# Kernel optimization log

Measured on AMD Instinct MI355X. Metric: run time of the kernel, lower is better.

Reference implementation:

```python
import jax, jax.numpy as jnp
import numpy as np

B, C, N, K = 32, 1024, 2048, 64


def fps_indices(x, num):
    """Farthest-feature sampling. x: (B, N, C). Returns int32 indices (B, num).
    Deterministic start at index 0 (standard PointNet++ style loop)."""
    b, n, _ = x.shape

    def step(carry, _):
        dists, farthest = carry
        centroid = jnp.take_along_axis(x, farthest[:, None, None], axis=1)  # (B,1,C)
        d = jnp.sum((x - centroid) ** 2, axis=-1)  # (B,N)
        dists = jnp.minimum(dists, d)
        nxt = jnp.argmax(dists, axis=1).astype(jnp.int32)
        return (dists, nxt), farthest

    init = (jnp.full((b, n), 1e10, x.dtype), jnp.zeros((b,), jnp.int32))
    _, idx = jax.lax.scan(step, init, None, length=num)
    return idx.T  # (B, num)


def conv1x1(w, bias, x):
    # w: (out,in), x: (B,in,n) -> (B,out,n)
    return jnp.einsum('oi,bin->bon', w, x) + bias[:, None]


def setup_inputs() -> dict:
    key = jax.random.key(0)
    ks = jax.random.split(key, 16)
    s = 0.02
    return {
        'point_feat': jax.random.normal(ks[0], (B, C, N), jnp.float32),
        'global_feat': jax.random.normal(ks[1], (B, C), jnp.float32),
        'ps1_w': jax.random.normal(ks[2], (C, 128, K), jnp.float32) * s,
        'ps1_b': jnp.zeros((128,), jnp.float32),
        'm1c1_w': jax.random.normal(ks[3], (128, 2 * C + 128), jnp.float32) * s,
        'm1c1_b': jnp.zeros((128,), jnp.float32),
        'm1c2_w': jax.random.normal(ks[4], (128, 128), jnp.float32) * s,
        'm1c2_b': jnp.zeros((128,), jnp.float32),
        'm1sc_w': jax.random.normal(ks[5], (128, 2 * C + 128), jnp.float32) * s,
        'm1sc_b': jnp.zeros((128,), jnp.float32),
        'm2c1_w': jax.random.normal(ks[6], (64, 128), jnp.float32) * s,
        'm2c1_b': jnp.zeros((64,), jnp.float32),
        'm2c2_w': jax.random.normal(ks[7], (3, 64), jnp.float32) * s,
        'm2c2_b': jnp.zeros((3,), jnp.float32),
    }


def reference(point_feat, global_feat, ps1_w, ps1_b, m1c1_w, m1c1_b,
              m1c2_w, m1c2_b, m1sc_w, m1sc_b, m2c1_w, m2c1_b, m2c2_w, m2c2_b):
    # ffs: farthest-feature sample + gather
    xt = jnp.transpose(point_feat, (0, 2, 1))            # (B,N,C)
    idx = fps_indices(xt, K)                             # (B,K)
    feat_ffs = jnp.take_along_axis(xt, idx[:, :, None], axis=1)  # (B,K,C)
    feat_ffs = jnp.transpose(feat_ffs, (0, 2, 1))        # (B,C,K)

    # ConvTranspose1d on a length-1 input == outer product with kernel
    x1 = jnp.einsum('bi,iok->bok', global_feat, ps1_w) + ps1_b[:, None]  # (B,128,K)

    gf = jnp.broadcast_to(global_feat[:, :, None], (B, C, K))
    cat = jnp.concatenate([x1, feat_ffs, gf], axis=1)    # (B,2176,K)

    # MLP_Res
    shortcut = conv1x1(m1sc_w, m1sc_b, cat)
    h = conv1x1(m1c2_w, m1c2_b, jax.nn.relu(conv1x1(m1c1_w, m1c1_b, cat))) + shortcut

    # mlp_2
    pred = conv1x1(m2c2_w, m2c2_b, jax.nn.relu(conv1x1(m2c1_w, m2c1_b, h)))  # (B,3,K)
    return jnp.transpose(pred, (0, 2, 1))                # (B,K,3)
```

## Files before the change

### kernel.cpp

```cpp
#include <hip/hip_runtime.h>

#define BB_ 32
#define CC_ 1024
#define NN_ 2048
#define KK_ 64

typedef __bf16 bf16x8 __attribute__((ext_vector_type(8)));
typedef __bf16 bf16x2 __attribute__((ext_vector_type(2)));
typedef float f32x4 __attribute__((ext_vector_type(4)));
typedef unsigned int u32;

__device__ inline unsigned short f2bf_rn(float f) {
    unsigned u = __float_as_uint(f);
    unsigned r = (u + 0x7fffu + ((u >> 16) & 1u)) >> 16;
    return (unsigned short)r;
}

__device__ inline unsigned pack_bf16_rn(float f0, float f1) {
#if __has_builtin(__builtin_amdgcn_cvt_pk_bf16_f32)
    union { bf16x2 v; unsigned u; } x;
    x.v = __builtin_amdgcn_cvt_pk_bf16_f32(f0, f1);
    return x.u;
#else
    return (unsigned)f2bf_rn(f0) | ((unsigned)f2bf_rn(f1) << 16);
#endif
}

__device__ inline void gload16(const void* g, void* l) {
    __builtin_amdgcn_global_load_lds(
        (const __attribute__((address_space(1))) u32*)g,
        (__attribute__((address_space(3))) u32*)l, 16, 0, 0);
}

__device__ void convert_body(const float* __restrict__ X,
                             unsigned char* __restrict__ Xc, int g0,
                             int cid, int t) {
    int chunk = cid & 7;
    int kt = (cid >> 3) & 31;
    int lb = cid >> 8;
    int n = chunk * 256 + t;
    int b = g0 + lb;
    const float* Xb = X + (size_t)b * CC_ * NN_;
    unsigned char* dst = Xc + (((size_t)lb * 32 + kt) * NN_ + n) * 128;
    int sw = n & 7;
#pragma unroll
    for (int q = 0; q < 4; q++) {
        float f[8];
#pragma unroll
        for (int j = 0; j < 8; j++)
            f[j] = Xb[(size_t)(kt * 32 + q * 8 + j) * NN_ + n];
        union { unsigned u[4]; uint4 v; } hq, lq;
#pragma unroll
        for (int j2 = 0; j2 < 4; j2++) {
            float a = f[2 * j2], c = f[2 * j2 + 1];
            unsigned hp = pack_bf16_rn(a, c);
            float h0f = __uint_as_float((hp & 0xffffu) << 16);
            float h1f = __uint_as_float(hp & 0xffff0000u);
            hq.u[j2] = hp;
            lq.u[j2] = pack_bf16_rn(a - h0f, c - h1f);
        }
        int p = q ^ sw;
        *(uint4*)(dst + (p << 4)) = hq.v;
        *(uint4*)(dst + ((p ^ 4) << 4)) = lq.v;
    }
}

__global__ void convert_kernel(const float* __restrict__ X,
                               unsigned char* __restrict__ Xc, int g0) {
    convert_body(X, Xc, g0, blockIdx.x, threadIdx.x);
}

__device__ void fps_block(const float* Gb, int* idx, int b) {
    __shared__ float swv[2][4];
    __shared__ int swi[2][4];
    int t = threadIdx.x;
    float dist[8], nr[8];
#pragma unroll
    for (int r = 0; r < 8; r++) {
        nr[r] = Gb[(size_t)(t + 256 * r) * (NN_ + 1)];
        dist[r] = 1e10f;
    }
    if (t == 0) idx[b * KK_] = 0;
    int far = 0;
    for (int k = 1; k < KK_; k++) {
        float nf = Gb[(size_t)far * (NN_ + 1)];
        const float* grow = Gb + (size_t)far * NN_;
        float v = -1.f;
        int pi = 0;
#pragma unroll
        for (int r = 0; r < 8; r++) {
            float d = nr[r] + nf - 2.f * grow[t + 256 * r];
            dist[r] = fminf(dist[r], d);
            if (dist[r] > v) { v = dist[r]; pi = t + 256 * r; }
        }
#pragma unroll
        for (int off = 32; off; off >>= 1) {
            float ov = __shfl_down(v, off);
            int oi = __shfl_down(pi, off);
            if (ov > v || (ov == v && oi < pi)) { v = ov; pi = oi; }
        }
        int par = k & 1;
        if ((t & 63) == 0) { swv[par][t >> 6] = v; swi[par][t >> 6] = pi; }
        __syncthreads();
        float bv = swv[par][0];
        int bi = swi[par][0];
#pragma unroll
        for (int ww = 1; ww < 4; ww++) {
            float wv2 = swv[par][ww]; int wi2 = swi[par][ww];
            if (wv2 > bv || (wv2 == bv && wi2 < bi)) { bv = wv2; bi = wi2; }
        }
        far = bi;
        if (t == 0) idx[b * KK_ + k] = bi;
    }
}

__global__ __launch_bounds__(256, 2) void gram_fps_kernel(
    const unsigned char* __restrict__ Xc, float* __restrict__ G,
    const float* Gprev, int* __restrict__ idx, int nFps, int g0prev,
    const float* __restrict__ X, unsigned char* __restrict__ XcNext,
    int g0next, int nGram, int gs) {
    int bx = (int)blockIdx.x;
    if (bx < nFps) {
        fps_block(Gprev + (size_t)bx * NN_ * NN_, idx, g0prev + bx);
        return;
    }
    bx -= nFps;
    if (bx >= nGram) {
        convert_body(X, XcNext, g0next, bx - nGram, threadIdx.x);
        return;
    }
    int lb = bx % gs;
    int tt = bx / gs;
    int tn = (int)((sqrtf(8.f * tt + 1.f) - 1.f) * 0.5f);
    while ((tn + 1) * (tn + 2) / 2 <= tt) tn++;
    while (tn * (tn + 1) / 2 > tt) tn--;
    int tm = tt - tn * (tn + 1) / 2;
    bool diag = (tm == tn);
    int t = threadIdx.x;
    __shared__ __align__(16) unsigned char sMem[128 * 132 * 4];

    const unsigned char* XcB = Xc + (size_t)lb * 32 * NN_ * 128;
    int w = t >> 6, l = t & 63;
    int m0w = (w & 1) * 64, n0w = (w >> 1) * 64;
    int q = l >> 4, rr = l & 15;

    f32x4 zero = {0.f, 0.f, 0.f, 0.f};
    f32x4 acc[4][4];
#pragma unroll
    for (int mt = 0; mt < 4; mt++)
#pragma unroll
        for (int nt = 0; nt < 4; nt++) acc[mt][nt] = zero;

    auto stage = [&](int buf, int kt) {
        const unsigned char* Ab = XcB + ((size_t)kt * NN_ + (size_t)tm * 128) * 128;
        const unsigned char* Bb = XcB + ((size_t)kt * NN_ + (size_t)tn * 128) * 128;
        unsigned char* dA = sMem + buf * 32768;
        unsigned char* dB = dA + 16384;
#pragma unroll
        for (int r = 0; r < 4; r++) {
            gload16(Ab + r * 4096 + t * 16, dA + r * 4096 + t * 16);
            gload16(Bb + r * 4096 + t * 16, dB + r * 4096 + t * 16);
        }
    };

    stage(0, 0);
    for (int kt = 0; kt < 32; kt++) {
        int c = kt & 1;
        if (kt < 31) {
            stage(c ^ 1, kt + 1);
            asm volatile("s_waitcnt vmcnt(8)" ::: "memory");
        } else {
            asm volatile("s_waitcnt vmcnt(0)" ::: "memory");
        }
        __builtin_amdgcn_sched_barrier(0);
        __builtin_amdgcn_s_barrier();

        const unsigned char* cA = sMem + c * 32768;
        const unsigned char* cB = cA + 16384;
        bf16x8 ah[4], al[4], bh[4], bl[4];
#pragma unroll
        for (int mt = 0; mt < 4; mt++) {
            int ra = m0w + mt * 16 + rr;
            int pa = q ^ (ra & 7);
            ah[mt] = *(const bf16x8*)(cA + ra * 128 + (pa << 4));
            al[mt] = *(const bf16x8*)(cA + ra * 128 + ((pa ^ 4) << 4));
            int rb = n0w + mt * 16 + rr;
            int pb = q ^ (rb & 7);
            bh[mt] = *(const bf16x8*)(cB + rb * 128 + (pb << 4));
            bl[mt] = *(const bf16x8*)(cB + rb * 128 + ((pb ^ 4) << 4));
        }
#pragma unroll
        for (int mt = 0; mt < 4; mt++)
#pragma unroll
            for (int nt = 0; nt < 4; nt++) {
                acc[mt][nt] = __builtin_amdgcn_mfma_f32_16x16x32_bf16(ah[mt], bh[nt], acc[mt][nt], 0, 0, 0);
                acc[mt][nt] = __builtin_amdgcn_mfma_f32_16x16x32_bf16(ah[mt], bl[nt], acc[mt][nt], 0, 0, 0);
                acc[mt][nt] = __builtin_amdgcn_mfma_f32_16x16x32_bf16(al[mt], bh[nt], acc[mt][nt], 0, 0, 0);
            }
        __builtin_amdgcn_s_barrier();
    }

    float* Gb = G + (size_t)lb * NN_ * NN_;
    int i0 = tm * 128, j0 = tn * 128;
    int cc = l & 15;
    float* tb = (float*)sMem;
#pragma unroll
    for (int mt = 0; mt < 4; mt++)
#pragma unroll
        for (int nt = 0; nt < 4; nt++)
#pragma unroll
            for (int r = 0; r < 4; r++) {
                int gi = m0w + mt * 16 + q * 4 + r;
                int gj = n0w + nt * 16 + cc;
                float val = acc[mt][nt][r];
                Gb[(size_t)(i0 + gi) * NN_ + j0 + gj] = val;
                if (!diag) tb[gj * 132 + gi] = val;
            }
    if (!diag) {
        __syncthreads();
#pragma unroll
        for (int m = 0; m < 16; m++) {
            int f = t + 256 * m;
            int jj = f >> 5, sg = f & 31;
            float4 v4 = *(const float4*)(tb + jj * 132 + sg * 4);
            *(float4*)(&Gb[(size_t)(j0 + jj) * NN_ + i0 + sg * 4]) = v4;
        }
    }
}

__global__ void x1_fps_kernel(const float* __restrict__ gf, const float* __restrict__ w,
                              const float* __restrict__ bias, float* __restrict__ cat,
                              const float* Gprev, int* __restrict__ idx,
                              int g0prev, int nFps) {
    if ((int)blockIdx.x < nFps) {
        fps_block(Gprev + (size_t)blockIdx.x * NN_ * NN_, idx, g0prev + blockIdx.x);
        return;
    }
    int bid = blockIdx.x - nFps;
    int t = threadIdx.x;
    int okg = bid & 31, bg = bid >> 5;
    int ok = okg * 256 + t;
    int o = ok >> 6, k = ok & 63;
    float acc[8];
#pragma unroll
    for (int j = 0; j < 8; j++) acc[j] = 0.f;
    const float* g = gf + (size_t)(bg * 8) * CC_;
    for (int i = 0; i < CC_; i++) {
        float wv = w[(size_t)(i * 128 + o) * KK_ + k];
#pragma unroll
        for (int j = 0; j < 8; j++) acc[j] += g[j * CC_ + i] * wv;
    }
    float bv = bias[o];
#pragma unroll
    for (int j = 0; j < 8; j++)
        cat[((size_t)(bg * 8 + j) * 2176 + o) * KK_ + k] = acc[j] + bv;
}

__global__ void catfill_kernel(const float* __restrict__ X, const float* __restrict__ gf,
                               const int* __restrict__ idx, float* __restrict__ cat) {
    int b = blockIdx.y;
    int t = threadIdx.x;
    int ch = 128 + blockIdx.x * 4 + (t >> 6);
    int k = t & 63;
    float v;
    if (ch < 1152) {
        int c = ch - 128;
        int ik = idx[b * KK_ + k];
        v = X[((size_t)b * CC_ + c) * NN_ + ik];
    } else {
        v = gf[b * CC_ + (ch - 1152)];
    }
    cat[((size_t)b * 2176 + ch) * KK_ + k] = v;
}

__global__ void mlp1_kernel(const float* __restrict__ cat, const float* __restrict__ w1,
                            const float* __restrict__ b1, const float* __restrict__ wsc,
                            const float* __restrict__ bsc, float* __restrict__ t1,
                            float* __restrict__ sc) {
    __shared__ float red[2][16][64];
    int b = blockIdx.y, og = blockIdx.x;
    int t = threadIdx.x;
    int k = t & 63, sub = t >> 6;
    int o0 = og * 4;
    const float* cb = cat + (size_t)b * 2176 * KK_;
    float a1[4], a2[4];
#pragma unroll
    for (int j = 0; j < 4; j++) { a1[j] = 0.f; a2[j] = 0.f; }
    int iBeg = sub * 544;
    int off = (b & 7) * 68;
#pragma unroll 1
    for (int seg = 0; seg < 2; seg++) {
        int s0 = iBeg + (seg ? 0 : off);
        int s1 = seg ? iBeg + off : iBeg + 544;
        for (int i = s0; i < s1; i += 4) {
            float v0 = cb[(i + 0) * KK_ + k];
            float v1 = cb[(i + 1) * KK_ + k];
            float v2 = cb[(i + 2) * KK_ + k];
            float v3 = cb[(i + 3) * KK_ + k];
#pragma unroll
            for (int j = 0; j < 4; j++) {
                float4 wv = *(const float4*)(w1 + (size_t)(o0 + j) * 2176 + i);
                a1[j] += wv.x * v0 + wv.y * v1 + wv.z * v2 + wv.w * v3;
                float4 ws = *(const float4*)(wsc + (size_t)(o0 + j) * 2176 + i);
                a2[j] += ws.x * v0 + ws.y * v1 + ws.z * v2 + ws.w * v3;
            }
        }
    }
#pragma unroll
    for (int j = 0; j < 4; j++) {
        red[0][sub * 4 + j][k] = a1[j];
        red[1][sub * 4 + j][k] = a2[j];
    }
    __syncthreads();
#pragma unroll
    for (int p = t; p < 512; p += 256) {
        int m = p >> 8;
        int j = (p >> 6) & 3;
        int kk = p & 63;
        float s = red[m][j][kk] + red[m][4 + j][kk] + red[m][8 + j][kk] + red[m][12 + j][kk];
        int o = o0 + j;
        size_t oidx = ((size_t)b * 128 + o) * KK_ + kk;
        if (m == 0) t1[oidx] = fmaxf(s + b1[o], 0.f);
        else        sc[oidx] = s + bsc[o];
    }
}

__global__ void mlp2_kernel(const float* __restrict__ t1, const float* __restrict__ sc,
                            const float* __restrict__ w2, const float* __restrict__ b2,
                            const float* __restrict__ w3, const float* __restrict__ b3,
                            const float* __restrict__ w4, const float* __restrict__ b4,
                            float* __restrict__ out) {
    __shared__ float sT[128 * 64];
    __shared__ float sH[128 * 64];
    __shared__ float sR[64 * 64];
    int b = blockIdx.x, t = threadIdx.x;
    const float4* t1b4 = (const float4*)(t1 + (size_t)b * 8192);
    for (int j = t; j < 2048; j += 256) ((float4*)sT)[j] = t1b4[j];
    __syncthreads();
    int k = t & 63, og = t >> 6;
    const float* scb = sc + (size_t)b * 8192;

#pragma unroll
    for (int pass = 0; pass < 4; pass++) {
        int o0 = og * 32 + pass * 8;
        float acc[8];
#pragma unroll
        for (int j = 0; j < 8; j++) acc[j] = b2[o0 + j] + scb[(o0 + j) * 64 + k];
        for (int i4 = 0; i4 < 32; i4++) {
            float v0 = sT[(i4 * 4 + 0) * 64 + k];
            float v1 = sT[(i4 * 4 + 1) * 64 + k];
            float v2 = sT[(i4 * 4 + 2) * 64 + k];
            float v3 = sT[(i4 * 4 + 3) * 64 + k];
#pragma unroll
            for (int j = 0; j < 8; j++) {
                float4 wv = *(const float4*)(w2 + (size_t)(o0 + j) * 128 + i4 * 4);
                acc[j] += wv.x * v0 + wv.y * v1 + wv.z * v2 + wv.w * v3;
            }
        }
#pragma unroll
        for (int j = 0; j < 8; j++) sH[(o0 + j) * 64 + k] = acc[j];
    }
    __syncthreads();

#pragma unroll
    for (int pass = 0; pass < 2; pass++) {
        int o0 = og * 16 + pass * 8;
        float acc[8];
#pragma unroll
        for (int j = 0; j < 8; j++) acc[j] = b3[o0 + j];
        for (int i4 = 0; i4 < 32; i4++) {
            float v0 = sH[(i4 * 4 + 0) * 64 + k];
            float v1 = sH[(i4 * 4 + 1) * 64 + k];
            float v2 = sH[(i4 * 4 + 2) * 64 + k];
            float v3 = sH[(i4 * 4 + 3) * 64 + k];
#pragma unroll
            for (int j = 0; j < 8; j++) {
                float4 wv = *(const float4*)(w3 + (size_t)(o0 + j) * 128 + i4 * 4);
                acc[j] += wv.x * v0 + wv.y * v1 + wv.z * v2 + wv.w * v3;
            }
        }
#pragma unroll
        for (int j = 0; j < 8; j++) sR[(o0 + j) * 64 + k] = fmaxf(acc[j], 0.f);
    }
    __syncthreads();

    if (t < 192) {
        int o = t % 3;
        int kk = t / 3;
        float a0 = 0.f, a1 = 0.f, a2 = 0.f, a3 = 0.f;
        for (int i4 = 0; i4 < 16; i4++) {
            float4 wv = *(const float4*)(w4 + o * 64 + i4 * 4);
            a0 += wv.x * sR[(i4 * 4 + 0) * 64 + kk];
            a1 += wv.y * sR[(i4 * 4 + 1) * 64 + kk];
            a2 += wv.z * sR[(i4 * 4 + 2) * 64 + kk];
            a3 += wv.w * sR[(i4 * 4 + 3) * 64 + kk];
        }
        out[((size_t)b * KK_ + kk) * 3 + o] = b4[o] + ((a0 + a1) + (a2 + a3));
    }
}

extern "C" void kernel_launch(void* const* d_in, const int* in_sizes, int n_in,
                              void* d_out, int out_size, void* d_ws, size_t ws_size,
                              hipStream_t stream) {
    const float* X    = (const float*)d_in[0];
    const float* gf   = (const float*)d_in[1];
    const float* ps1w = (const float*)d_in[2];
    const float* ps1b = (const float*)d_in[3];
    const float* w1   = (const float*)d_in[4];
    const float* b1   = (const float*)d_in[5];
    const float* w2   = (const float*)d_in[6];
    const float* b2   = (const float*)d_in[7];
    const float* wsc  = (const float*)d_in[8];
    const float* bscp = (const float*)d_in[9];
    const float* w3   = (const float*)d_in[10];
    const float* b3   = (const float*)d_in[11];
    const float* w4   = (const float*)d_in[12];
    const float* b4   = (const float*)d_in[13];
    float* out = (float*)d_out;

    const size_t G_PER  = (size_t)NN_ * NN_ * 4;
    const size_t XC_PER = (size_t)32 * NN_ * 128;
    const size_t IDX_B  = (size_t)BB_ * KK_ * 4;
    const size_t CAT_B  = (size_t)BB_ * 2176 * KK_ * 4;
    const size_t T1_B   = (size_t)BB_ * 128 * KK_ * 4;
    size_t rest = IDX_B + CAT_B + 2 * T1_B;

    int gs = 1, merged = 0, pipe = 0;
    {
        const int tg[8]  = {8, 8, 4, 4, 2, 2, 1, 1};
        const int tmg[8] = {1, 1, 1, 1, 1, 1, 1, 0};
        const int tp[8]  = {1, 0, 1, 0, 1, 0, 0, 0};
        for (int i = 0; i < 8; i++) {
            size_t need = (size_t)(tmg[i] ? 2 : 1) * tg[i] * G_PER
                        + (size_t)(tp[i] ? 2 : 1) * tg[i] * XC_PER + rest;
            if (ws_size >= need) { gs = tg[i]; merged = tmg[i]; pipe = tp[i]; break; }
        }
    }

    char* ws = (char*)d_ws;
    float* Gbuf = (float*)ws;
    size_t gBufBytes = (size_t)(merged ? 2 : 1) * gs * G_PER;
    unsigned char* Xc0 = (unsigned char*)(ws + gBufBytes);
    unsigned char* Xc1 = Xc0 + (pipe ? (size_t)gs * XC_PER : 0);
    char* p = (char*)Xc0 + (size_t)(pipe ? 2 : 1) * gs * XC_PER;
    int* idxws = (int*)p;    p += IDX_B;
    float* cat = (float*)p;  p += CAT_B;
    float* t1  = (float*)p;  p += T1_B;
    float* sc  = (float*)p;

    int ng = BB_ / gs;
    size_t halfElems = (size_t)gs * NN_ * NN_;
    int nGram = gs * 136;
    int nConvAll = 256 * gs;

    if (pipe) convert_kernel<<<nConvAll, 256, 0, stream>>>(X, Xc0, 0);
    for (int g = 0; g < ng; g++) {
        int g0 = g * gs;
        unsigned char* Xcur  = (g & 1) ? Xc1 : Xc0;
        unsigned char* Xnext = (g & 1) ? Xc0 : Xc1;
        if (!pipe) {
            Xcur = Xc0;
            convert_kernel<<<nConvAll, 256, 0, stream>>>(X, Xc0, g0);
        }
        float* Gcur = Gbuf + (merged ? (size_t)(g & 1) * halfElems : 0);
        float* Gprev = Gbuf + (merged ? (size_t)((g & 1) ^ 1) * halfElems : 0);
        int nFps = (merged && g > 0) ? gs : 0;
        int nConv = (pipe && g < ng - 1) ? nConvAll : 0;
        gram_fps_kernel<<<nFps + nGram + nConv, 256, 0, stream>>>(
            Xcur, Gcur, Gprev, idxws, nFps, g0 - gs, X, Xnext, g0 + gs, nGram, gs);
        if (!merged) {
            gram_fps_kernel<<<gs, 256, 0, stream>>>(
                Xcur, Gcur, Gcur, idxws, gs, g0, X, Xnext, 0, 0, gs);
        }
    }
    int nFpsLast = merged ? gs : 0;
    float* Glast = Gbuf + (merged ? (size_t)((ng - 1) & 1) * halfElems : 0);
    x1_fps_kernel<<<nFpsLast + 128, 256, 0, stream>>>(
        gf, ps1w, ps1b, cat, Glast, idxws, BB_ - gs, nFpsLast);
    catfill_kernel<<<dim3(512, BB_), 256, 0, stream>>>(X, gf, idxws, cat);
    mlp1_kernel<<<dim3(32, BB_), 256, 0, stream>>>(cat, w1, b1, wsc, bscp, t1, sc);
    mlp2_kernel<<<BB_, 256, 0, stream>>>(t1, sc, w2, b2, w3, b3, w4, b4, out);
}
```

Measured before the change: 1.306 ms.

## Move MLP_Res first layer onto split-bf16 MFMA with split-K partials

Replaces the scalar fp32 mlp1 kernel with a pipeline that converts weights and the concatenated activations into hi/lo bf16 pairs in swizzled tiles. An MFMA kernel then computes both the conv and shortcut GEMMs using four bf16 products per tile, split four ways over K, and a reduction kernel adds the partials, bias and ReLU. The aim is to replace slow scalar FMA work with matrix cores while keeping near-fp32 accuracy. The cost is three extra launches, extra traffic for the conversions and partial sums, and reuse of workspace scratch that is only taken when it is large enough.

```diff
diff --git a/kernel.cpp b/kernel.cpp
--- a/kernel.cpp
+++ b/kernel.cpp
@@ -24,6 +24,20 @@
 #else
     return (unsigned)f2bf_rn(f0) | ((unsigned)f2bf_rn(f1) << 16);
 #endif
+}
+
+__device__ inline void split8(const float* f, uint4* H, uint4* L) {
+    union { unsigned u[4]; uint4 v; } hq, lq;
+#pragma unroll
+    for (int j2 = 0; j2 < 4; j2++) {
+        float a = f[2 * j2], c = f[2 * j2 + 1];
+        unsigned hp = pack_bf16_rn(a, c);
+        float h0f = __uint_as_float((hp & 0xffffu) << 16);
+        float h1f = __uint_as_float(hp & 0xffff0000u);
+        hq.u[j2] = hp;
+        lq.u[j2] = pack_bf16_rn(a - h0f, c - h1f);
+    }
+    *H = hq.v; *L = lq.v;
 }
 
 __device__ inline void gload16(const void* g, void* l) {
@@ -49,19 +63,11 @@
 #pragma unroll
         for (int j = 0; j < 8; j++)
             f[j] = Xb[(size_t)(kt * 32 + q * 8 + j) * NN_ + n];
-        union { unsigned u[4]; uint4 v; } hq, lq;
-#pragma unroll
-        for (int j2 = 0; j2 < 4; j2++) {
-            float a = f[2 * j2], c = f[2 * j2 + 1];
-            unsigned hp = pack_bf16_rn(a, c);
-            float h0f = __uint_as_float((hp & 0xffffu) << 16);
-            float h1f = __uint_as_float(hp & 0xffff0000u);
-            hq.u[j2] = hp;
-            lq.u[j2] = pack_bf16_rn(a - h0f, c - h1f);
-        }
+        uint4 hq, lq;
+        split8(f, &hq, &lq);
         int p = q ^ sw;
-        *(uint4*)(dst + (p << 4)) = hq.v;
-        *(uint4*)(dst + ((p ^ 4) << 4)) = lq.v;
+        *(uint4*)(dst + (p << 4)) = hq;
+        *(uint4*)(dst + ((p ^ 4) << 4)) = lq;
     }
 }
 
@@ -271,6 +277,140 @@
         v = gf[b * CC_ + (ch - 1152)];
     }
     cat[((size_t)b * 2176 + ch) * KK_ + k] = v;
+}
+
+__global__ void wconv_kernel(const float* __restrict__ w1, const float* __restrict__ wsc,
+                             unsigned char* __restrict__ Wc) {
+    int it = blockIdx.x;
+    int m = threadIdx.x;
+    const float* src = (m < 128 ? w1 + (size_t)m * 2176
+                                : wsc + (size_t)(m - 128) * 2176) + it * 32;
+    unsigned char* dst = Wc + ((size_t)it * 256 + m) * 128;
+    int sw = m & 7;
+#pragma unroll
+    for (int q = 0; q < 4; q++) {
+        float f[8];
+        *(float4*)f       = *(const float4*)(src + q * 8);
+        *(float4*)(f + 4) = *(const float4*)(src + q * 8 + 4);
+        uint4 hq, lq;
+        split8(f, &hq, &lq);
+        int p = q ^ sw;
+        *(uint4*)(dst + (p << 4)) = hq;
+        *(uint4*)(dst + ((p ^ 4) << 4)) = lq;
+    }
+}
+
+__global__ void cconv_kernel(const float* __restrict__ cat,
+                             unsigned char* __restrict__ Cc) {
+    int it = blockIdx.x, b = blockIdx.y;
+    int t = threadIdx.x;
+    int k = t & 63, q = t >> 6;
+    const float* src = cat + (size_t)b * 2176 * KK_ + (size_t)(it * 32 + q * 8) * KK_ + k;
+    float f[8];
+#pragma unroll
+    for (int j = 0; j < 8; j++) f[j] = src[j * KK_];
+    uint4 hq, lq;
+    split8(f, &hq, &lq);
+    unsigned char* dst = Cc + (((size_t)b * 68 + it) * 64 + k) * 128;
+    int p = q ^ (k & 7);
+    *(uint4*)(dst + (p << 4)) = hq;
+    *(uint4*)(dst + ((p ^ 4) << 4)) = lq;
+}
+
+__global__ __launch_bounds__(256, 2) void mlp1m_kernel(
+    const unsigned char* __restrict__ Wc, const unsigned char* __restrict__ Cc,
+    float* __restrict__ P) {
+    int s = blockIdx.x & 3, b = blockIdx.x >> 2;
+    int t = threadIdx.x;
+    __shared__ __align__(16) unsigned char sMem[2 * 40960];
+    int w = t >> 6, l = t & 63;
+    int m0w = w * 64;
+    int q = l >> 4, rr = l & 15;
+    const unsigned char* WcS = Wc + (size_t)s * 17 * 32768;
+    const unsigned char* CcS = Cc + ((size_t)b * 68 + s * 17) * 8192;
+
+    f32x4 zero = {0.f, 0.f, 0.f, 0.f};
+    f32x4 acc[4][4];
+#pragma unroll
+    for (int mt = 0; mt < 4; mt++)
+#pragma unroll
+        for (int nt = 0; nt < 4; nt++) acc[mt][nt] = zero;
+
+    auto stage = [&](int buf, int kt) {
+        const unsigned char* A = WcS + (size_t)kt * 32768;
+        const unsigned char* Bc = CcS + (size_t)kt * 8192;
+        unsigned char* dA = sMem + buf * 40960;
+        unsigned char* dB = dA + 32768;
+#pragma unroll
+        for (int r = 0; r < 8; r++)
+            gload16(A + r * 4096 + t * 16, dA + r * 4096 + t * 16);
+#pragma unroll
+        for (int r = 0; r < 2; r++)
+            gload16(Bc + r * 4096 + t * 16, dB + r * 4096 + t * 16);
+    };
+
+    stage(0, 0);
+    for (int kt = 0; kt < 17; kt++) {
+        int c = kt & 1;
+        if (kt < 16) {
+            stage(c ^ 1, kt + 1);
+            asm volatile("s_waitcnt vmcnt(10)" ::: "memory");
+        } else {
+            asm volatile("s_waitcnt vmcnt(0)" ::: "memory");
+        }
+        __builtin_amdgcn_sched_barrier(0);
+        __builtin_amdgcn_s_barrier();
+
+        const unsigned char* cA = sMem + c * 40960;
+        const unsigned char* cB = cA + 32768;
+        bf16x8 ah[4], al[4], bh[4], bl[4];
+#pragma unroll
+        for (int mt = 0; mt < 4; mt++) {
+            int ra = m0w + mt * 16 + rr;
+            int pa = q ^ (ra & 7);
+            ah[mt] = *(const bf16x8*)(cA + ra * 128 + (pa << 4));
+            al[mt] = *(const bf16x8*)(cA + ra * 128 + ((pa ^ 4) << 4));
+            int rb = mt * 16 + rr;
+            int pb = q ^ (rb & 7);
+            bh[mt] = *(const bf16x8*)(cB + rb * 128 + (pb << 4));
+            bl[mt] = *(const bf16x8*)(cB + rb * 128 + ((pb ^ 4) << 4));
+        }
+#pragma unroll
+        for (int mt = 0; mt < 4; mt++)
+#pragma unroll
+            for (int nt = 0; nt < 4; nt++) {
+                acc[mt][nt] = __builtin_amdgcn_mfma_f32_16x16x32_bf16(ah[mt], bh[nt], acc[mt][nt], 0, 0, 0);
+                acc[mt][nt] = __builtin_amdgcn_mfma_f32_16x16x32_bf16(ah[mt], bl[nt], acc[mt][nt], 0, 0, 0);
+                acc[mt][nt] = __builtin_amdgcn_mfma_f32_16x16x32_bf16(al[mt], bh[nt], acc[mt][nt], 0, 0, 0);
+                acc[mt][nt] = __builtin_amdgcn_mfma_f32_16x16x32_bf16(al[mt], bl[nt], acc[mt][nt], 0, 0, 0);
+            }
+        __builtin_amdgcn_s_barrier();
+    }
+
+    float* Pb = P + (size_t)(s * 32 + b) * 256 * 64;
+    int cc = l & 15;
+#pragma unroll
+    for (int mt = 0; mt < 4; mt++)
+#pragma unroll
+        for (int nt = 0; nt < 4; nt++)
+#pragma unroll
+            for (int r = 0; r < 4; r++) {
+                int gi = m0w + mt * 16 + q * 4 + r;
+                int gj = nt * 16 + cc;
+                Pb[(size_t)gi * 64 + gj] = acc[mt][nt][r];
+            }
+}
+
+__global__ void mred_kernel(const float* __restrict__ P, const float* __restrict__ b1,
+                            const float* __restrict__ bsc, float* __restrict__ t1,
+                            float* __restrict__ sc) {
+    int pid = (int)blockIdx.x * 256 + threadIdx.x;
+    int k = pid & 63, o = (pid >> 6) & 255, b = pid >> 14;
+    const size_t SLAB = (size_t)32 * 256 * 64;
+    size_t base = ((size_t)b * 256 + o) * 64 + k;
+    float sum = P[base] + P[base + SLAB] + P[base + 2 * SLAB] + P[base + 3 * SLAB];
+    if (o < 128) t1[((size_t)b * 128 + o) * KK_ + k] = fmaxf(sum + b1[o], 0.f);
+    else         sc[((size_t)b * 128 + (o - 128)) * KK_ + k] = sum + bsc[o - 128];
 }
 
 __global__ void mlp1_kernel(const float* __restrict__ cat, const float* __restrict__ w1,
@@ -442,11 +582,19 @@
     size_t gBufBytes = (size_t)(merged ? 2 : 1) * gs * G_PER;
     unsigned char* Xc0 = (unsigned char*)(ws + gBufBytes);
     unsigned char* Xc1 = Xc0 + (pipe ? (size_t)gs * XC_PER : 0);
-    char* p = (char*)Xc0 + (size_t)(pipe ? 2 : 1) * gs * XC_PER;
+    size_t xcBytes = (size_t)(pipe ? 2 : 1) * gs * XC_PER;
+    char* p = (char*)Xc0 + xcBytes;
     int* idxws = (int*)p;    p += IDX_B;
     float* cat = (float*)p;  p += CAT_B;
     float* t1  = (float*)p;  p += T1_B;
     float* sc  = (float*)p;
+
+    const size_t WC_B = (size_t)68 * 256 * 128;
+    const size_t CC_B = (size_t)BB_ * 68 * 64 * 128;
+    const size_t P_B  = (size_t)4 * BB_ * 256 * 64 * 4;
+    char* scratch = nullptr;
+    if (xcBytes >= WC_B + CC_B + P_B) scratch = (char*)Xc0;
+    else if (gBufBytes >= WC_B + CC_B + P_B) scratch = (char*)Gbuf;
 
     int ng = BB_ / gs;
     size_t halfElems = (size_t)gs * NN_ * NN_;
@@ -478,6 +626,16 @@
     x1_fps_kernel<<<nFpsLast + 128, 256, 0, stream>>>(
         gf, ps1w, ps1b, cat, Glast, idxws, BB_ - gs, nFpsLast);
     catfill_kernel<<<dim3(512, BB_), 256, 0, stream>>>(X, gf, idxws, cat);
-    mlp1_kernel<<<dim3(32, BB_), 256, 0, stream>>>(cat, w1, b1, wsc, bscp, t1, sc);
+    if (scratch) {
+        unsigned char* Wc = (unsigned char*)scratch;
+        unsigned char* Cc = Wc + WC_B;
+        float* P = (float*)(Cc + CC_B);
+        wconv_kernel<<<68, 256, 0, stream>>>(w1, wsc, Wc);
+        cconv_kernel<<<dim3(68, BB_), 256, 0, stream>>>(cat, Cc);
+        mlp1m_kernel<<<128, 256, 0, stream>>>(Wc, Cc, P);
+        mred_kernel<<<2048, 256, 0, stream>>>(P, b1, bscp, t1, sc);
+    } else {
+        mlp1_kernel<<<dim3(32, BB_), 256, 0, stream>>>(cat, w1, b1, wsc, bscp, t1, sc);
+    }
     mlp2_kernel<<<BB_, 256, 0, stream>>>(t1, sc, w2, b2, w3, b3, w4, b4, out);
 }
```

Result: faster. 1.177 ms (-9.9%).
